# Optimization experiments

Hardware: AMD Instinct MI355X
Metric: run time of the kernel (lower is better)

Reference implementation:

```python
import jax, jax.numpy as jnp
import numpy as np

B, N, IN_C, HID_C, OUT_C = 8, 2048, 128, 256, 32


def setup_inputs() -> dict:
    key = jax.random.key(0)
    ks = jax.random.split(key, 8)
    s1 = 1.0 / np.sqrt(IN_C)
    s2 = 1.0 / np.sqrt(HID_C)
    return {
        "x": jax.random.normal(ks[0], (B, N, IN_C), dtype=jnp.float32),
        "A": jax.random.randint(ks[1], (B, N, N), 0, 2, dtype=jnp.int32),
        "W1_l": jax.random.normal(ks[2], (IN_C, HID_C), dtype=jnp.float32) * s1,
        "W1_r": jax.random.normal(ks[3], (IN_C, HID_C), dtype=jnp.float32) * s1,
        "b1": jnp.zeros((HID_C,), dtype=jnp.float32),
        "W2_l": jax.random.normal(ks[4], (HID_C, OUT_C), dtype=jnp.float32) * s2,
        "W2_r": jax.random.normal(ks[5], (HID_C, OUT_C), dtype=jnp.float32) * s2,
        "b2": jnp.zeros((OUT_C,), dtype=jnp.float32),
    }


def _mean_agg(mask, deg_inv, h):
    # edge (i, j) means source i -> target j (PyG source_to_target flow):
    # agg[b, j] = mean over i with A[b, i, j] != 0 of h[b, i]
    return jnp.einsum("bij,bid->bjd", mask, h) * deg_inv


def reference(x, A, W1_l, W1_r, b1, W2_l, W2_r, b2):
    mask = (A != 0).astype(x.dtype)            # [B, N, N]
    deg = jnp.sum(mask, axis=1)                # in-degree per target node, [B, N]
    deg_inv = (1.0 / jnp.maximum(deg, 1.0))[..., None]  # isolated nodes -> 0 agg

    # SAGEConv 1: lin_l(mean_agg(x)) + lin_r(x) + bias, then ReLU
    # (dropout p=0.2 is inactive in eval mode)
    h = _mean_agg(mask, deg_inv, x) @ W1_l + x @ W1_r + b1
    h = jax.nn.relu(h)

    # SAGEConv 2
    out = _mean_agg(mask, deg_inv, h) @ W2_l + h @ W2_r + b2  # [B, N, OUT_C]
    return (jax.nn.log_softmax(out, axis=-1), out)
```

## Files before the change

kernel.cpp:

```cpp
#include <hip/hip_runtime.h>


#define B_   8
#define N_   2048
#define INC  128
#define HID  256
#define OUTC 32

typedef __bf16 bf16;
typedef __attribute__((ext_vector_type(8))) __bf16 bf16x8;
typedef __attribute__((ext_vector_type(4))) float f32x4;
typedef __attribute__((ext_vector_type(4))) unsigned int u32x4;
typedef __attribute__((ext_vector_type(2))) unsigned int u32x2;

__device__ __forceinline__ unsigned short f2bf(float f) {
  unsigned int u = __float_as_uint(f);
  u += 0x7FFFu + ((u >> 16) & 1u);
  return (unsigned short)(u >> 16);
}

__device__ __forceinline__ f32x4 mfma16(bf16x8 a, bf16x8 b, f32x4 c) {
  return __builtin_amdgcn_mfma_f32_16x16x32_bf16(a, b, c, 0, 0, 0);
}

__device__ __forceinline__ bf16x8 ones_frag() {
  union { unsigned short u[8]; bf16x8 v; } o;
#pragma unroll
  for (int i = 0; i < 8; i++) o.u[i] = 0x3F80;
  return o.v;
}

__global__ __launch_bounds__(256) void k_pack_w(
    const float* __restrict__ W1l, const float* __restrict__ W1r,
    const float* __restrict__ W2l, const float* __restrict__ W2r,
    unsigned short* __restrict__ W1cT, unsigned short* __restrict__ W2cT) {
  int idx = blockIdx.x * 256 + threadIdx.x;
  {
    int e = idx >> 8, k = idx & 255;
    float v = (k < 128) ? W1l[k * 256 + e] : W1r[(k - 128) * 256 + e];
    W1cT[idx] = f2bf(v);
  }
  if (idx < 32 * 512) {
    int c = idx >> 9, k = idx & 511;
    float v = (k < 256) ? W2l[k * 32 + c] : W2r[(k - 256) * 32 + c];
    W2cT[idx] = f2bf(v);
  }
}

__global__ __launch_bounds__(512) void k_agg1(
    const int* __restrict__ A, const float* __restrict__ x,
    unsigned short* __restrict__ agg1, float* __restrict__ deg_inv) {
#define KP 40
  __shared__ __align__(16) unsigned short mts[64 * KP];
  __shared__ __align__(16) unsigned short xts[INC * KP];
  const int b = blockIdx.y;
  const int j0 = blockIdx.x * 64;
  const int t = threadIdx.x;
  const int w = t >> 6, l = t & 63;
  const int wj = w & 3, wd = w >> 2;
  const int lr = l & 15, lq = l >> 4;

  const f32x4 zero = {0.f, 0.f, 0.f, 0.f};
  f32x4 acc[4] = {zero, zero, zero, zero};
  f32x4 dacc = zero;
  const bf16x8 onesf = ones_frag();

  const int sj = t & 63;
  const int si4 = (t >> 6) << 2;
  const int* Ab = A + (size_t)b * N_ * N_ + j0 + sj;
  const int sd = t & 127;
  const int si8 = (t >> 7) << 3;
  const float* xb = x + (size_t)b * N_ * INC + sd;

  for (int k0 = 0; k0 < N_; k0 += 32) {
    __syncthreads();
    {
      const int* ap = Ab + (size_t)(k0 + si4) * N_;
      int a0 = ap[0], a1 = ap[N_], a2 = ap[2 * N_], a3 = ap[3 * N_];
      u32x2 p;
      p.x = (a0 ? 0x3F80u : 0u) | ((a1 ? 0x3F80u : 0u) << 16);
      p.y = (a2 ? 0x3F80u : 0u) | ((a3 ? 0x3F80u : 0u) << 16);
      *reinterpret_cast<u32x2*>(&mts[sj * KP + si4]) = p;
    }
    {
      const float* xp = xb + (size_t)(k0 + si8) * INC;
      u32x4 p;
#pragma unroll
      for (int q = 0; q < 4; q++) {
        unsigned int lo = f2bf(xp[(2 * q) * INC]);
        unsigned int hi = f2bf(xp[(2 * q + 1) * INC]);
        p[q] = lo | (hi << 16);
      }
      *reinterpret_cast<u32x4*>(&xts[sd * KP + si8]) = p;
    }
    __syncthreads();
    bf16x8 af = *reinterpret_cast<const bf16x8*>(&mts[(wj * 16 + lr) * KP + lq * 8]);
    dacc = mfma16(af, onesf, dacc);
#pragma unroll
    for (int ds = 0; ds < 4; ds++) {
      bf16x8 bfr = *reinterpret_cast<const bf16x8*>(&xts[(wd * 64 + ds * 16 + lr) * KP + lq * 8]);
      acc[ds] = mfma16(af, bfr, acc[ds]);
    }
  }

  float dinv[4];
#pragma unroll
  for (int r = 0; r < 4; r++) dinv[r] = 1.0f / fmaxf(dacc[r], 1.0f);
  if (wd == 0 && lr == 0) {
#pragma unroll
    for (int r = 0; r < 4; r++)
      deg_inv[b * N_ + j0 + wj * 16 + lq * 4 + r] = dinv[r];
  }
  unsigned short* ag = agg1 + ((size_t)b * N_ + j0) * INC;
#pragma unroll
  for (int ds = 0; ds < 4; ds++)
#pragma unroll
    for (int r = 0; r < 4; r++) {
      int j = wj * 16 + lq * 4 + r;
      int d = wd * 64 + ds * 16 + lr;
      ag[(size_t)j * INC + d] = f2bf(acc[ds][r] * dinv[r]);
    }
#undef KP
}

__global__ __launch_bounds__(512) void k_dense1(
    const unsigned short* __restrict__ agg1, const float* __restrict__ x,
    const unsigned short* __restrict__ W1cT, const float* __restrict__ b1,
    unsigned short* __restrict__ h) {
  __shared__ __align__(16) unsigned short acat[64 * 264];
  const int b = blockIdx.y;
  const int j0 = blockIdx.x * 64;
  const int t = threadIdx.x;
  const int w = t >> 6, l = t & 63;
  const int wj = w & 3, we = w >> 2;
  const int lr = l & 15, lq = l >> 4;

  {
    const int sj = t >> 3, seg = t & 7;
    u32x4* dst = reinterpret_cast<u32x4*>(&acat[sj * 264 + seg * 32]);
    if (seg < 4) {
      const u32x4* src = reinterpret_cast<const u32x4*>(
          agg1 + ((size_t)(b * N_ + j0 + sj)) * INC + seg * 32);
#pragma unroll
      for (int q = 0; q < 4; q++) dst[q] = src[q];
    } else {
      const float* src = x + ((size_t)(b * N_ + j0 + sj)) * INC + (seg - 4) * 32;
#pragma unroll
      for (int q = 0; q < 4; q++) {
        u32x4 p;
#pragma unroll
        for (int e = 0; e < 4; e++) {
          unsigned int lo = f2bf(src[q * 8 + 2 * e]);
          unsigned int hi = f2bf(src[q * 8 + 2 * e + 1]);
          p[e] = lo | (hi << 16);
        }
        dst[q] = p;
      }
    }
  }
  __syncthreads();

  const f32x4 zero = {0.f, 0.f, 0.f, 0.f};
  f32x4 acc[8] = {zero, zero, zero, zero, zero, zero, zero, zero};
#pragma unroll
  for (int ks = 0; ks < 8; ks++) {
    bf16x8 af = *reinterpret_cast<const bf16x8*>(&acat[(wj * 16 + lr) * 264 + ks * 32 + lq * 8]);
#pragma unroll
    for (int es = 0; es < 8; es++) {
      bf16x8 bfr = *reinterpret_cast<const bf16x8*>(
          W1cT + (we * 128 + es * 16 + lr) * 256 + ks * 32 + lq * 8);
      acc[es] = mfma16(af, bfr, acc[es]);
    }
  }

  unsigned short* hB = h + ((size_t)b * N_ + j0) * HID;
#pragma unroll
  for (int es = 0; es < 8; es++) {
    int e = we * 128 + es * 16 + lr;
    float bias = b1[e];
#pragma unroll
    for (int r = 0; r < 4; r++) {
      int j = wj * 16 + lq * 4 + r;
      float v = fmaxf(acc[es][r] + bias, 0.0f);
      hB[(size_t)j * HID + e] = f2bf(v);
    }
  }
}

__global__ __launch_bounds__(512) void k_agg2(
    const int* __restrict__ A, const unsigned short* __restrict__ h,
    const float* __restrict__ deg_inv, unsigned short* __restrict__ agg2) {
#define KP 40
  __shared__ __align__(16) unsigned short mts[64 * KP];
  __shared__ __align__(16) unsigned short hts[HID * KP];
  const int b = blockIdx.y;
  const int j0 = blockIdx.x * 64;
  const int t = threadIdx.x;
  const int w = t >> 6, l = t & 63;
  const int wj = w & 3, we = w >> 2;
  const int lr = l & 15, lq = l >> 4;

  const f32x4 zero = {0.f, 0.f, 0.f, 0.f};
  f32x4 acc[8] = {zero, zero, zero, zero, zero, zero, zero, zero};

  const int sj = t & 63;
  const int si4 = (t >> 6) << 2;
  const int* Ab = A + (size_t)b * N_ * N_ + j0 + sj;
  const int se2 = (t & 127) * 2;
  const int si8 = (t >> 7) << 3;
  const unsigned short* hb = h + (size_t)b * N_ * HID + se2;

  for (int k0 = 0; k0 < N_; k0 += 32) {
    __syncthreads();
    {
      const int* ap = Ab + (size_t)(k0 + si4) * N_;
      int a0 = ap[0], a1 = ap[N_], a2 = ap[2 * N_], a3 = ap[3 * N_];
      u32x2 p;
      p.x = (a0 ? 0x3F80u : 0u) | ((a1 ? 0x3F80u : 0u) << 16);
      p.y = (a2 ? 0x3F80u : 0u) | ((a3 ? 0x3F80u : 0u) << 16);
      *reinterpret_cast<u32x2*>(&mts[sj * KP + si4]) = p;
    }
    {
      const unsigned short* hp = hb + (size_t)(k0 + si8) * HID;
      unsigned int vv[8];
#pragma unroll
      for (int q = 0; q < 8; q++)
        vv[q] = *reinterpret_cast<const unsigned int*>(hp + (size_t)q * HID);
      u32x4 p0, p1;
#pragma unroll
      for (int q4 = 0; q4 < 4; q4++) {
        p0[q4] = (vv[2 * q4] & 0xFFFFu) | ((vv[2 * q4 + 1] & 0xFFFFu) << 16);
        p1[q4] = (vv[2 * q4] >> 16) | ((vv[2 * q4 + 1] >> 16) << 16);
      }
      *reinterpret_cast<u32x4*>(&hts[se2 * KP + si8]) = p0;
      *reinterpret_cast<u32x4*>(&hts[(se2 + 1) * KP + si8]) = p1;
    }
    __syncthreads();
    bf16x8 af = *reinterpret_cast<const bf16x8*>(&mts[(wj * 16 + lr) * KP + lq * 8]);
#pragma unroll
    for (int es = 0; es < 8; es++) {
      bf16x8 bfr = *reinterpret_cast<const bf16x8*>(&hts[(we * 128 + es * 16 + lr) * KP + lq * 8]);
      acc[es] = mfma16(af, bfr, acc[es]);
    }
  }

  float dinv[4];
#pragma unroll
  for (int r = 0; r < 4; r++)
    dinv[r] = deg_inv[b * N_ + j0 + wj * 16 + lq * 4 + r];
  unsigned short* ag = agg2 + ((size_t)b * N_ + j0) * HID;
#pragma unroll
  for (int es = 0; es < 8; es++) {
    int e = we * 128 + es * 16 + lr;
#pragma unroll
    for (int r = 0; r < 4; r++) {
      int j = wj * 16 + lq * 4 + r;
      ag[(size_t)j * HID + e] = f2bf(acc[es][r] * dinv[r]);
    }
  }
#undef KP
}

__global__ __launch_bounds__(256) void k_out(
    const unsigned short* __restrict__ agg2, const unsigned short* __restrict__ h,
    const unsigned short* __restrict__ W2cT, const float* __restrict__ b2,
    float* __restrict__ out) {
  __shared__ __align__(16) unsigned short acat[64 * 136];
  const int b = blockIdx.y;
  const int j0 = blockIdx.x * 64;
  const int t = threadIdx.x;
  const int w = t >> 6, l = t & 63;
  const int lr = l & 15, lq = l >> 4;
  const int wj = w;

  const f32x4 zero = {0.f, 0.f, 0.f, 0.f};
  f32x4 acc[2] = {zero, zero};

  const int sj = t >> 2, seg = t & 3;
  const unsigned short* a2B = agg2 + (size_t)b * N_ * HID;
  const unsigned short* hB = h + (size_t)b * N_ * HID;

  for (int kc = 0; kc < 4; kc++) {
    __syncthreads();
    {
      int kcol = kc * 128 + seg * 32;
      const unsigned short* src = (kcol < 256)
          ? (a2B + (size_t)(j0 + sj) * HID + kcol)
          : (hB + (size_t)(j0 + sj) * HID + (kcol - 256));
      u32x4* dst = reinterpret_cast<u32x4*>(&acat[sj * 136 + seg * 32]);
      const u32x4* s4 = reinterpret_cast<const u32x4*>(src);
#pragma unroll
      for (int q = 0; q < 4; q++) dst[q] = s4[q];
    }
    __syncthreads();
#pragma unroll
    for (int ks = 0; ks < 4; ks++) {
      bf16x8 af = *reinterpret_cast<const bf16x8*>(&acat[(wj * 16 + lr) * 136 + ks * 32 + lq * 8]);
#pragma unroll
      for (int cs = 0; cs < 2; cs++) {
        bf16x8 bfr = *reinterpret_cast<const bf16x8*>(
            W2cT + (cs * 16 + lr) * 512 + kc * 128 + ks * 32 + lq * 8);
        acc[cs] = mfma16(af, bfr, acc[cs]);
      }
    }
  }

  float v[2][4];
#pragma unroll
  for (int cs = 0; cs < 2; cs++) {
    float bias = b2[cs * 16 + lr];
#pragma unroll
    for (int r = 0; r < 4; r++) v[cs][r] = acc[cs][r] + bias;
  }
#pragma unroll
  for (int r = 0; r < 4; r++) {
    float m = fmaxf(v[0][r], v[1][r]);
    for (int d = 1; d < 16; d <<= 1) m = fmaxf(m, __shfl_xor(m, d, 64));
    float s = __expf(v[0][r] - m) + __expf(v[1][r] - m);
    for (int d = 1; d < 16; d <<= 1) s += __shfl_xor(s, d, 64);
    float ls = m + __logf(s);
    int j = j0 + wj * 16 + lq * 4 + r;
    size_t base = ((size_t)b * N_ + j) * OUTC;
#pragma unroll
    for (int cs = 0; cs < 2; cs++) {
      out[base + cs * 16 + lr] = v[cs][r] - ls;
      out[(size_t)B_ * N_ * OUTC + base + cs * 16 + lr] = v[cs][r];
    }
  }
}

extern "C" void kernel_launch(void* const* d_in, const int* in_sizes, int n_in,
                              void* d_out, int out_size, void* d_ws, size_t ws_size,
                              hipStream_t stream) {
  (void)in_sizes; (void)n_in; (void)out_size; (void)ws_size;
  const float* x   = (const float*)d_in[0];
  const int*   A   = (const int*)d_in[1];
  const float* W1l = (const float*)d_in[2];
  const float* W1r = (const float*)d_in[3];
  const float* b1  = (const float*)d_in[4];
  const float* W2l = (const float*)d_in[5];
  const float* W2r = (const float*)d_in[6];
  const float* b2  = (const float*)d_in[7];
  float* out = (float*)d_out;

  char* ws = (char*)d_ws;
  unsigned short* W1cT    = (unsigned short*)(ws + 0);
  unsigned short* W2cT    = (unsigned short*)(ws + 131072);
  float*          deg_inv = (float*)(ws + 163840);
  unsigned short* agg1    = (unsigned short*)(ws + 229376);
  unsigned short* h       = (unsigned short*)(ws + 4423680);
  unsigned short* agg2    = (unsigned short*)(ws + 12812288);

  k_pack_w<<<dim3(256), dim3(256), 0, stream>>>(W1l, W1r, W2l, W2r, W1cT, W2cT);
  k_agg1  <<<dim3(32, 8), dim3(512), 0, stream>>>(A, x, agg1, deg_inv);
  k_dense1<<<dim3(32, 8), dim3(512), 0, stream>>>(agg1, x, W1cT, b1, h);
  k_agg2  <<<dim3(32, 8), dim3(512), 0, stream>>>(A, h, deg_inv, agg2);
  k_out   <<<dim3(32, 8), dim3(256), 0, stream>>>(agg2, h, W2cT, b2, out);
}
```

Before: 330.8 us.

## Bit-pack adjacency, reassociate layer-2 weights before aggregation, drop LDS staging

The int32 adjacency is read once and packed into a bitmask, which both aggregation kernels reuse. Each packed byte is expanded into MFMA A-fragments through a small LUT, so A is no longer read twice at 4 bytes per entry. Layer 2 applies W2_l to h before aggregating, shrinking the second aggregation from 256 to 32 channels, and fuses the log-softmax into it. x is pre-transposed to bf16 so the aggregation loops read fragments directly from global memory without LDS or barriers. The cost is extra prep kernels and more rounding from bf16 hl being aggregated instead of h.

New measurement: 431.2 us. +30.3%, slower.

```diff
diff --git a/kernel.cpp b/kernel.cpp
--- a/kernel.cpp
+++ b/kernel.cpp
@@ -7,7 +7,6 @@
 #define HID  256
 #define OUTC 32
 
-typedef __bf16 bf16;
 typedef __attribute__((ext_vector_type(8))) __bf16 bf16x8;
 typedef __attribute__((ext_vector_type(4))) float f32x4;
 typedef __attribute__((ext_vector_type(4))) unsigned int u32x4;
@@ -30,302 +29,268 @@
   return o.v;
 }
 
-__global__ __launch_bounds__(256) void k_pack_w(
+__global__ __launch_bounds__(256) void k_prep_bits(
+    const int* __restrict__ A, unsigned int* __restrict__ bits) {
+  __shared__ unsigned int tl[256 * 17];
+  const int b = blockIdx.y;
+  const int js = blockIdx.x & 7, isp = blockIdx.x >> 3;
+  const int j0 = js * 256, ib = isp * 512;
+  const int t = threadIdx.x;
+  const int* Ab = A + ((size_t)b * N_ + ib) * N_ + j0 + t;
+
+  for (int q = 0; q < 16; q++) {
+    unsigned int wv = 0;
+    const int* ap = Ab + (size_t)q * 32 * N_;
+#pragma unroll
+    for (int bit = 0; bit < 32; bit++)
+      wv |= (ap[(size_t)bit * N_] != 0 ? 1u : 0u) << bit;
+    tl[t * 17 + q] = wv;
+  }
+  __syncthreads();
+  unsigned int* bout = bits + ((size_t)b * N_ + j0) * 64 + (ib >> 5);
+#pragma unroll
+  for (int k = 0; k < 16; k++) {
+    int g = k * 256 + t;
+    int jl = g >> 4, q = g & 15;
+    bout[(size_t)jl * 64 + q] = tl[jl * 17 + q];
+  }
+}
+
+__global__ __launch_bounds__(256) void k_prep_small(
+    const float* __restrict__ x,
     const float* __restrict__ W1l, const float* __restrict__ W1r,
     const float* __restrict__ W2l, const float* __restrict__ W2r,
+    unsigned short* __restrict__ xT, unsigned short* __restrict__ acat1,
     unsigned short* __restrict__ W1cT, unsigned short* __restrict__ W2cT) {
-  int idx = blockIdx.x * 256 + threadIdx.x;
-  {
-    int e = idx >> 8, k = idx & 255;
-    float v = (k < 128) ? W1l[k * 256 + e] : W1r[(k - 128) * 256 + e];
-    W1cT[idx] = f2bf(v);
-  }
-  if (idx < 32 * 512) {
-    int c = idx >> 9, k = idx & 511;
-    float v = (k < 256) ? W2l[k * 32 + c] : W2r[(k - 256) * 32 + c];
-    W2cT[idx] = f2bf(v);
-  }
-}
-
-__global__ __launch_bounds__(512) void k_agg1(
-    const int* __restrict__ A, const float* __restrict__ x,
-    unsigned short* __restrict__ agg1, float* __restrict__ deg_inv) {
-#define KP 40
-  __shared__ __align__(16) unsigned short mts[64 * KP];
-  __shared__ __align__(16) unsigned short xts[INC * KP];
-  const int b = blockIdx.y;
-  const int j0 = blockIdx.x * 64;
-  const int t = threadIdx.x;
-  const int w = t >> 6, l = t & 63;
-  const int wj = w & 3, wd = w >> 2;
-  const int lr = l & 15, lq = l >> 4;
+  const int bx = blockIdx.x, t = threadIdx.x;
+  if (bx < 256) {
+    __shared__ unsigned short xls[128 * 72];
+    const int b = bx >> 5, it = bx & 31, i0 = it * 64;
+    const int dq = (t & 31) * 4;
+    const int irow = t >> 5;
+#pragma unroll
+    for (int s = 0; s < 8; s++) {
+      int il = s * 8 + irow;
+      int i = i0 + il;
+      f32x4 v = *reinterpret_cast<const f32x4*>(x + ((size_t)(b * N_ + i)) * INC + dq);
+      unsigned int p0 = f2bf(v[0]) | ((unsigned int)f2bf(v[1]) << 16);
+      unsigned int p1 = f2bf(v[2]) | ((unsigned int)f2bf(v[3]) << 16);
+      u32x2 pk = {p0, p1};
+      *reinterpret_cast<u32x2*>(acat1 + ((size_t)(b * N_ + i)) * HID + 128 + dq) = pk;
+      xls[(dq + 0) * 72 + il] = f2bf(v[0]);
+      xls[(dq + 1) * 72 + il] = f2bf(v[1]);
+      xls[(dq + 2) * 72 + il] = f2bf(v[2]);
+      xls[(dq + 3) * 72 + il] = f2bf(v[3]);
+    }
+    __syncthreads();
+    const int d = t >> 1, half = t & 1;
+    const u32x4* src = reinterpret_cast<const u32x4*>(&xls[d * 72 + half * 32]);
+    u32x4* dst = reinterpret_cast<u32x4*>(xT + ((size_t)(b * INC + d)) * N_ + i0 + half * 32);
+#pragma unroll
+    for (int q = 0; q < 4; q++) dst[q] = src[q];
+  } else if (bx < 320) {
+    int base = (bx - 256) * 1024 + t * 4;
+#pragma unroll
+    for (int q = 0; q < 4; q++) {
+      int id = base + q;
+      int e = id >> 8, k = id & 255;
+      float v = (k < 128) ? W1l[k * 256 + e] : W1r[(k - 128) * 256 + e];
+      W1cT[id] = f2bf(v);
+    }
+  } else {
+    int base = (bx - 320) * 1024 + t * 4;
+#pragma unroll
+    for (int q = 0; q < 4; q++) {
+      int id = base + q;
+      int n = id >> 8, k = id & 255;
+      float v = (n < 32) ? W2l[k * 32 + n] : W2r[k * 32 + (n - 32)];
+      W2cT[id] = f2bf(v);
+    }
+  }
+}
+
+__global__ __launch_bounds__(256) void k_agg1(
+    const unsigned int* __restrict__ bits, const unsigned short* __restrict__ xT,
+    unsigned short* __restrict__ acat1, float* __restrict__ deg_inv) {
+  __shared__ u32x2 lut[16];
+  const int t = threadIdx.x;
+  if (t < 16) {
+    unsigned int w0 = (t & 1 ? 0x3F80u : 0u) | (t & 2 ? 0x3F800000u : 0u);
+    unsigned int w1 = (t & 4 ? 0x3F80u : 0u) | (t & 8 ? 0x3F800000u : 0u);
+    u32x2 e = {w0, w1};
+    lut[t] = e;
+  }
+  __syncthreads();
+  const int w = t >> 6, l = t & 63, lr = l & 15, lq = l >> 4;
+  const int b = blockIdx.y;
+  const int j0w = blockIdx.x * 64 + w * 16;
+  const unsigned int* bp = bits + ((size_t)(b * N_ + j0w + lr)) * 64;
+  const unsigned short* xb = xT + (size_t)b * INC * N_;
+
+  const f32x4 zero = {0.f, 0.f, 0.f, 0.f};
+  f32x4 acc[8] = {zero, zero, zero, zero, zero, zero, zero, zero};
+  f32x4 dacc = zero;
+  const bf16x8 onesf = ones_frag();
+
+  for (int k0 = 0; k0 < N_; k0 += 32) {
+    unsigned int w32 = bp[k0 >> 5];
+    unsigned int bval = (w32 >> (lq * 8)) & 0xFFu;
+    union { u32x2 u2[2]; bf16x8 v; } af;
+    af.u2[0] = lut[bval & 15u];
+    af.u2[1] = lut[bval >> 4];
+    dacc = mfma16(af.v, onesf, dacc);
+#pragma unroll
+    for (int ds = 0; ds < 8; ds++) {
+      bf16x8 bfr = *reinterpret_cast<const bf16x8*>(
+          xb + ((size_t)(ds * 16 + lr)) * N_ + k0 + lq * 8);
+      acc[ds] = mfma16(af.v, bfr, acc[ds]);
+    }
+  }
+
+  float dinv[4];
+#pragma unroll
+  for (int r = 0; r < 4; r++) dinv[r] = 1.0f / fmaxf(dacc[r], 1.0f);
+  if (lr == 0) {
+#pragma unroll
+    for (int r = 0; r < 4; r++)
+      deg_inv[b * N_ + j0w + lq * 4 + r] = dinv[r];
+  }
+  unsigned short* ag = acat1 + ((size_t)(b * N_ + j0w)) * HID;
+#pragma unroll
+  for (int ds = 0; ds < 8; ds++)
+#pragma unroll
+    for (int r = 0; r < 4; r++)
+      ag[(size_t)(lq * 4 + r) * HID + ds * 16 + lr] = f2bf(acc[ds][r] * dinv[r]);
+}
+
+__global__ __launch_bounds__(256) void k_dense1(
+    const unsigned short* __restrict__ acat1, const unsigned short* __restrict__ W1cT,
+    const float* __restrict__ b1, unsigned short* __restrict__ h) {
+  const int t = threadIdx.x;
+  const int w = t >> 6, l = t & 63, lr = l & 15, lq = l >> 4;
+  const int b = blockIdx.y;
+  const int jt = blockIdx.x >> 1, eh = blockIdx.x & 1;
+  const int j0w = jt * 64 + w * 16, e0 = eh * 128;
+  const unsigned short* ab = acat1 + ((size_t)(b * N_ + j0w + lr)) * HID;
+
+  const f32x4 zero = {0.f, 0.f, 0.f, 0.f};
+  f32x4 acc[8] = {zero, zero, zero, zero, zero, zero, zero, zero};
+#pragma unroll
+  for (int ks = 0; ks < 8; ks++) {
+    bf16x8 af = *reinterpret_cast<const bf16x8*>(ab + ks * 32 + lq * 8);
+#pragma unroll
+    for (int es = 0; es < 8; es++) {
+      bf16x8 bfr = *reinterpret_cast<const bf16x8*>(
+          W1cT + ((size_t)(e0 + es * 16 + lr)) * HID + ks * 32 + lq * 8);
+      acc[es] = mfma16(af, bfr, acc[es]);
+    }
+  }
+  unsigned short* hB = h + ((size_t)(b * N_ + j0w)) * HID;
+#pragma unroll
+  for (int es = 0; es < 8; es++) {
+    int e = e0 + es * 16 + lr;
+    float bias = b1[e];
+#pragma unroll
+    for (int r = 0; r < 4; r++)
+      hB[(size_t)(lq * 4 + r) * HID + e] = f2bf(fmaxf(acc[es][r] + bias, 0.0f));
+  }
+}
+
+__global__ __launch_bounds__(256) void k_hl(
+    const unsigned short* __restrict__ h, const unsigned short* __restrict__ W2cT,
+    const float* __restrict__ b2, unsigned short* __restrict__ hlT,
+    float* __restrict__ hr) {
+  const int t = threadIdx.x;
+  const int w = t >> 6, l = t & 63, lr = l & 15, lq = l >> 4;
+  const int b = blockIdx.y;
+  const int i0w = blockIdx.x * 64 + w * 16;
+  const unsigned short* hb = h + ((size_t)(b * N_ + i0w + lr)) * HID;
 
   const f32x4 zero = {0.f, 0.f, 0.f, 0.f};
   f32x4 acc[4] = {zero, zero, zero, zero};
-  f32x4 dacc = zero;
-  const bf16x8 onesf = ones_frag();
-
-  const int sj = t & 63;
-  const int si4 = (t >> 6) << 2;
-  const int* Ab = A + (size_t)b * N_ * N_ + j0 + sj;
-  const int sd = t & 127;
-  const int si8 = (t >> 7) << 3;
-  const float* xb = x + (size_t)b * N_ * INC + sd;
-
-  for (int k0 = 0; k0 < N_; k0 += 32) {
-    __syncthreads();
-    {
-      const int* ap = Ab + (size_t)(k0 + si4) * N_;
-      int a0 = ap[0], a1 = ap[N_], a2 = ap[2 * N_], a3 = ap[3 * N_];
-      u32x2 p;
-      p.x = (a0 ? 0x3F80u : 0u) | ((a1 ? 0x3F80u : 0u) << 16);
-      p.y = (a2 ? 0x3F80u : 0u) | ((a3 ? 0x3F80u : 0u) << 16);
-      *reinterpret_cast<u32x2*>(&mts[sj * KP + si4]) = p;
-    }
-    {
-      const float* xp = xb + (size_t)(k0 + si8) * INC;
-      u32x4 p;
-#pragma unroll
-      for (int q = 0; q < 4; q++) {
-        unsigned int lo = f2bf(xp[(2 * q) * INC]);
-        unsigned int hi = f2bf(xp[(2 * q + 1) * INC]);
-        p[q] = lo | (hi << 16);
-      }
-      *reinterpret_cast<u32x4*>(&xts[sd * KP + si8]) = p;
-    }
-    __syncthreads();
-    bf16x8 af = *reinterpret_cast<const bf16x8*>(&mts[(wj * 16 + lr) * KP + lq * 8]);
-    dacc = mfma16(af, onesf, dacc);
-#pragma unroll
-    for (int ds = 0; ds < 4; ds++) {
-      bf16x8 bfr = *reinterpret_cast<const bf16x8*>(&xts[(wd * 64 + ds * 16 + lr) * KP + lq * 8]);
-      acc[ds] = mfma16(af, bfr, acc[ds]);
-    }
-  }
-
-  float dinv[4];
-#pragma unroll
-  for (int r = 0; r < 4; r++) dinv[r] = 1.0f / fmaxf(dacc[r], 1.0f);
-  if (wd == 0 && lr == 0) {
+#pragma unroll
+  for (int ks = 0; ks < 8; ks++) {
+    bf16x8 af = *reinterpret_cast<const bf16x8*>(hb + ks * 32 + lq * 8);
+#pragma unroll
+    for (int ns = 0; ns < 4; ns++) {
+      bf16x8 bfr = *reinterpret_cast<const bf16x8*>(
+          W2cT + ((size_t)(ns * 16 + lr)) * HID + ks * 32 + lq * 8);
+      acc[ns] = mfma16(af, bfr, acc[ns]);
+    }
+  }
+#pragma unroll
+  for (int ns = 0; ns < 2; ns++) {
+    int c = ns * 16 + lr;
+    unsigned int p0 = f2bf(acc[ns][0]) | ((unsigned int)f2bf(acc[ns][1]) << 16);
+    unsigned int p1 = f2bf(acc[ns][2]) | ((unsigned int)f2bf(acc[ns][3]) << 16);
+    u32x2 pk = {p0, p1};
+    *reinterpret_cast<u32x2*>(hlT + ((size_t)(b * 32 + c)) * N_ + i0w + lq * 4) = pk;
+  }
+#pragma unroll
+  for (int ns = 2; ns < 4; ns++) {
+    int c = (ns - 2) * 16 + lr;
+    float bias = b2[c];
 #pragma unroll
     for (int r = 0; r < 4; r++)
-      deg_inv[b * N_ + j0 + wj * 16 + lq * 4 + r] = dinv[r];
-  }
-  unsigned short* ag = agg1 + ((size_t)b * N_ + j0) * INC;
-#pragma unroll
-  for (int ds = 0; ds < 4; ds++)
-#pragma unroll
-    for (int r = 0; r < 4; r++) {
-      int j = wj * 16 + lq * 4 + r;
-      int d = wd * 64 + ds * 16 + lr;
-      ag[(size_t)j * INC + d] = f2bf(acc[ds][r] * dinv[r]);
-    }
-#undef KP
-}
-
-__global__ __launch_bounds__(512) void k_dense1(
-    const unsigned short* __restrict__ agg1, const float* __restrict__ x,
-    const unsigned short* __restrict__ W1cT, const float* __restrict__ b1,
-    unsigned short* __restrict__ h) {
-  __shared__ __align__(16) unsigned short acat[64 * 264];
-  const int b = blockIdx.y;
-  const int j0 = blockIdx.x * 64;
-  const int t = threadIdx.x;
-  const int w = t >> 6, l = t & 63;
-  const int wj = w & 3, we = w >> 2;
-  const int lr = l & 15, lq = l >> 4;
-
-  {
-    const int sj = t >> 3, seg = t & 7;
-    u32x4* dst = reinterpret_cast<u32x4*>(&acat[sj * 264 + seg * 32]);
-    if (seg < 4) {
-      const u32x4* src = reinterpret_cast<const u32x4*>(
-          agg1 + ((size_t)(b * N_ + j0 + sj)) * INC + seg * 32);
-#pragma unroll
-      for (int q = 0; q < 4; q++) dst[q] = src[q];
-    } else {
-      const float* src = x + ((size_t)(b * N_ + j0 + sj)) * INC + (seg - 4) * 32;
-#pragma unroll
-      for (int q = 0; q < 4; q++) {
-        u32x4 p;
-#pragma unroll
-        for (int e = 0; e < 4; e++) {
-          unsigned int lo = f2bf(src[q * 8 + 2 * e]);
-          unsigned int hi = f2bf(src[q * 8 + 2 * e + 1]);
-          p[e] = lo | (hi << 16);
-        }
-        dst[q] = p;
-      }
-    }
+      hr[((size_t)(b * N_ + i0w + lq * 4 + r)) * OUTC + c] = acc[ns][r] + bias;
+  }
+}
+
+__global__ __launch_bounds__(256) void k_agg2out(
+    const unsigned int* __restrict__ bits, const unsigned short* __restrict__ hlT,
+    const float* __restrict__ deg_inv, const float* __restrict__ hr,
+    float* __restrict__ out) {
+  __shared__ u32x2 lut[16];
+  const int t = threadIdx.x;
+  if (t < 16) {
+    unsigned int w0 = (t & 1 ? 0x3F80u : 0u) | (t & 2 ? 0x3F800000u : 0u);
+    unsigned int w1 = (t & 4 ? 0x3F80u : 0u) | (t & 8 ? 0x3F800000u : 0u);
+    u32x2 e = {w0, w1};
+    lut[t] = e;
   }
   __syncthreads();
-
-  const f32x4 zero = {0.f, 0.f, 0.f, 0.f};
-  f32x4 acc[8] = {zero, zero, zero, zero, zero, zero, zero, zero};
-#pragma unroll
-  for (int ks = 0; ks < 8; ks++) {
-    bf16x8 af = *reinterpret_cast<const bf16x8*>(&acat[(wj * 16 + lr) * 264 + ks * 32 + lq * 8]);
-#pragma unroll
-    for (int es = 0; es < 8; es++) {
-      bf16x8 bfr = *reinterpret_cast<const bf16x8*>(
-          W1cT + (we * 128 + es * 16 + lr) * 256 + ks * 32 + lq * 8);
-      acc[es] = mfma16(af, bfr, acc[es]);
-    }
-  }
-
-  unsigned short* hB = h + ((size_t)b * N_ + j0) * HID;
-#pragma unroll
-  for (int es = 0; es < 8; es++) {
-    int e = we * 128 + es * 16 + lr;
-    float bias = b1[e];
-#pragma unroll
-    for (int r = 0; r < 4; r++) {
-      int j = wj * 16 + lq * 4 + r;
-      float v = fmaxf(acc[es][r] + bias, 0.0f);
-      hB[(size_t)j * HID + e] = f2bf(v);
-    }
-  }
-}
-
-__global__ __launch_bounds__(512) void k_agg2(
-    const int* __restrict__ A, const unsigned short* __restrict__ h,
-    const float* __restrict__ deg_inv, unsigned short* __restrict__ agg2) {
-#define KP 40
-  __shared__ __align__(16) unsigned short mts[64 * KP];
-  __shared__ __align__(16) unsigned short hts[HID * KP];
-  const int b = blockIdx.y;
-  const int j0 = blockIdx.x * 64;
-  const int t = threadIdx.x;
-  const int w = t >> 6, l = t & 63;
-  const int wj = w & 3, we = w >> 2;
-  const int lr = l & 15, lq = l >> 4;
-
-  const f32x4 zero = {0.f, 0.f, 0.f, 0.f};
-  f32x4 acc[8] = {zero, zero, zero, zero, zero, zero, zero, zero};
-
-  const int sj = t & 63;
-  const int si4 = (t >> 6) << 2;
-  const int* Ab = A + (size_t)b * N_ * N_ + j0 + sj;
-  const int se2 = (t & 127) * 2;
-  const int si8 = (t >> 7) << 3;
-  const unsigned short* hb = h + (size_t)b * N_ * HID + se2;
-
-  for (int k0 = 0; k0 < N_; k0 += 32) {
-    __syncthreads();
-    {
-      const int* ap = Ab + (size_t)(k0 + si4) * N_;
-      int a0 = ap[0], a1 = ap[N_], a2 = ap[2 * N_], a3 = ap[3 * N_];
-      u32x2 p;
-      p.x = (a0 ? 0x3F80u : 0u) | ((a1 ? 0x3F80u : 0u) << 16);
-      p.y = (a2 ? 0x3F80u : 0u) | ((a3 ? 0x3F80u : 0u) << 16);
-      *reinterpret_cast<u32x2*>(&mts[sj * KP + si4]) = p;
-    }
-    {
-      const unsigned short* hp = hb + (size_t)(k0 + si8) * HID;
-      unsigned int vv[8];
-#pragma unroll
-      for (int q = 0; q < 8; q++)
-        vv[q] = *reinterpret_cast<const unsigned int*>(hp + (size_t)q * HID);
-      u32x4 p0, p1;
-#pragma unroll
-      for (int q4 = 0; q4 < 4; q4++) {
-        p0[q4] = (vv[2 * q4] & 0xFFFFu) | ((vv[2 * q4 + 1] & 0xFFFFu) << 16);
-        p1[q4] = (vv[2 * q4] >> 16) | ((vv[2 * q4 + 1] >> 16) << 16);
-      }
-      *reinterpret_cast<u32x4*>(&hts[se2 * KP + si8]) = p0;
-      *reinterpret_cast<u32x4*>(&hts[(se2 + 1) * KP + si8]) = p1;
-    }
-    __syncthreads();
-    bf16x8 af = *reinterpret_cast<const bf16x8*>(&mts[(wj * 16 + lr) * KP + lq * 8]);
-#pragma unroll
-    for (int es = 0; es < 8; es++) {
-      bf16x8 bfr = *reinterpret_cast<const bf16x8*>(&hts[(we * 128 + es * 16 + lr) * KP + lq * 8]);
-      acc[es] = mfma16(af, bfr, acc[es]);
-    }
-  }
-
-  float dinv[4];
-#pragma unroll
-  for (int r = 0; r < 4; r++)
-    dinv[r] = deg_inv[b * N_ + j0 + wj * 16 + lq * 4 + r];
-  unsigned short* ag = agg2 + ((size_t)b * N_ + j0) * HID;
-#pragma unroll
-  for (int es = 0; es < 8; es++) {
-    int e = we * 128 + es * 16 + lr;
-#pragma unroll
-    for (int r = 0; r < 4; r++) {
-      int j = wj * 16 + lq * 4 + r;
-      ag[(size_t)j * HID + e] = f2bf(acc[es][r] * dinv[r]);
-    }
-  }
-#undef KP
-}
-
-__global__ __launch_bounds__(256) void k_out(
-    const unsigned short* __restrict__ agg2, const unsigned short* __restrict__ h,
-    const unsigned short* __restrict__ W2cT, const float* __restrict__ b2,
-    float* __restrict__ out) {
-  __shared__ __align__(16) unsigned short acat[64 * 136];
-  const int b = blockIdx.y;
-  const int j0 = blockIdx.x * 64;
-  const int t = threadIdx.x;
-  const int w = t >> 6, l = t & 63;
-  const int lr = l & 15, lq = l >> 4;
-  const int wj = w;
+  const int w = t >> 6, l = t & 63, lr = l & 15, lq = l >> 4;
+  const int b = blockIdx.y;
+  const int j0w = blockIdx.x * 64 + w * 16;
+  const unsigned int* bp = bits + ((size_t)(b * N_ + j0w + lr)) * 64;
+  const unsigned short* hb = hlT + (size_t)b * 32 * N_;
 
   const f32x4 zero = {0.f, 0.f, 0.f, 0.f};
   f32x4 acc[2] = {zero, zero};
 
-  const int sj = t >> 2, seg = t & 3;
-  const unsigned short* a2B = agg2 + (size_t)b * N_ * HID;
-  const unsigned short* hB = h + (size_t)b * N_ * HID;
-
-  for (int kc = 0; kc < 4; kc++) {
-    __syncthreads();
-    {
-      int kcol = kc * 128 + seg * 32;
-      const unsigned short* src = (kcol < 256)
-          ? (a2B + (size_t)(j0 + sj) * HID + kcol)
-          : (hB + (size_t)(j0 + sj) * HID + (kcol - 256));
-      u32x4* dst = reinterpret_cast<u32x4*>(&acat[sj * 136 + seg * 32]);
-      const u32x4* s4 = reinterpret_cast<const u32x4*>(src);
-#pragma unroll
-      for (int q = 0; q < 4; q++) dst[q] = s4[q];
-    }
-    __syncthreads();
-#pragma unroll
-    for (int ks = 0; ks < 4; ks++) {
-      bf16x8 af = *reinterpret_cast<const bf16x8*>(&acat[(wj * 16 + lr) * 136 + ks * 32 + lq * 8]);
-#pragma unroll
-      for (int cs = 0; cs < 2; cs++) {
-        bf16x8 bfr = *reinterpret_cast<const bf16x8*>(
-            W2cT + (cs * 16 + lr) * 512 + kc * 128 + ks * 32 + lq * 8);
-        acc[cs] = mfma16(af, bfr, acc[cs]);
-      }
-    }
-  }
-
-  float v[2][4];
-#pragma unroll
-  for (int cs = 0; cs < 2; cs++) {
-    float bias = b2[cs * 16 + lr];
-#pragma unroll
-    for (int r = 0; r < 4; r++) v[cs][r] = acc[cs][r] + bias;
-  }
+  for (int k0 = 0; k0 < N_; k0 += 32) {
+    unsigned int w32 = bp[k0 >> 5];
+    unsigned int bval = (w32 >> (lq * 8)) & 0xFFu;
+    union { u32x2 u2[2]; bf16x8 v; } af;
+    af.u2[0] = lut[bval & 15u];
+    af.u2[1] = lut[bval >> 4];
+#pragma unroll
+    for (int cs = 0; cs < 2; cs++) {
+      bf16x8 bfr = *reinterpret_cast<const bf16x8*>(
+          hb + ((size_t)(cs * 16 + lr)) * N_ + k0 + lq * 8);
+      acc[cs] = mfma16(af.v, bfr, acc[cs]);
+    }
+  }
+
+  const size_t SZ = (size_t)B_ * N_ * OUTC;
 #pragma unroll
   for (int r = 0; r < 4; r++) {
-    float m = fmaxf(v[0][r], v[1][r]);
+    int j = j0w + lq * 4 + r;
+    float dv = deg_inv[b * N_ + j];
+    size_t base = ((size_t)(b * N_ + j)) * OUTC;
+    float v0 = acc[0][r] * dv + hr[base + lr];
+    float v1 = acc[1][r] * dv + hr[base + 16 + lr];
+    float m = fmaxf(v0, v1);
+#pragma unroll
     for (int d = 1; d < 16; d <<= 1) m = fmaxf(m, __shfl_xor(m, d, 64));
-    float s = __expf(v[0][r] - m) + __expf(v[1][r] - m);
+    float s = __expf(v0 - m) + __expf(v1 - m);
+#pragma unroll
     for (int d = 1; d < 16; d <<= 1) s += __shfl_xor(s, d, 64);
     float ls = m + __logf(s);
-    int j = j0 + wj * 16 + lq * 4 + r;
-    size_t base = ((size_t)b * N_ + j) * OUTC;
-#pragma unroll
-    for (int cs = 0; cs < 2; cs++) {
-      out[base + cs * 16 + lr] = v[cs][r] - ls;
-      out[(size_t)B_ * N_ * OUTC + base + cs * 16 + lr] = v[cs][r];
-    }
+    out[base + lr] = v0 - ls;
+    out[base + 16 + lr] = v1 - ls;
+    out[SZ + base + lr] = v0;
+    out[SZ + base + 16 + lr] = v1;
   }
 }
 
@@ -347,13 +312,18 @@
   unsigned short* W1cT    = (unsigned short*)(ws + 0);
   unsigned short* W2cT    = (unsigned short*)(ws + 131072);
   float*          deg_inv = (float*)(ws + 163840);
-  unsigned short* agg1    = (unsigned short*)(ws + 229376);
+  unsigned int*   bits    = (unsigned int*)(ws + 229376);
+  unsigned short* xT      = (unsigned short*)(ws + 4423680);
   unsigned short* h       = (unsigned short*)(ws + 4423680);
-  unsigned short* agg2    = (unsigned short*)(ws + 12812288);
-
-  k_pack_w<<<dim3(256), dim3(256), 0, stream>>>(W1l, W1r, W2l, W2r, W1cT, W2cT);
-  k_agg1  <<<dim3(32, 8), dim3(512), 0, stream>>>(A, x, agg1, deg_inv);
-  k_dense1<<<dim3(32, 8), dim3(512), 0, stream>>>(agg1, x, W1cT, b1, h);
-  k_agg2  <<<dim3(32, 8), dim3(512), 0, stream>>>(A, h, deg_inv, agg2);
-  k_out   <<<dim3(32, 8), dim3(256), 0, stream>>>(agg2, h, W2cT, b2, out);
-}
+  unsigned short* acat1   = (unsigned short*)(ws + 12812288);
+  unsigned short* hlT     = (unsigned short*)(ws + 12812288);
+  float*          hr      = (float*)(ws + 13860864);
+
+  k_prep_bits <<<dim3(32, 8), dim3(256), 0, stream>>>(A, bits);
+  k_prep_small<<<dim3(336),   dim3(256), 0, stream>>>(x, W1l, W1r, W2l, W2r,
+                                                      xT, acat1, W1cT, W2cT);
+  k_agg1      <<<dim3(32, 8), dim3(256), 0, stream>>>(bits, xT, acat1, deg_inv);
+  k_dense1    <<<dim3(64, 8), dim3(256), 0, stream>>>(acat1, W1cT, b1, h);
+  k_hl        <<<dim3(32, 8), dim3(256), 0, stream>>>(h, W2cT, b2, hlT, hr);
+  k_agg2out   <<<dim3(32, 8), dim3(256), 0, stream>>>(bits, hlT, deg_inv, hr, out);
+}
```
